# Kernel optimization log

Measured on AMD Instinct MI355X. Metric: run time of the kernel, lower is better.

## Reference

```python
import jax, jax.numpy as jnp
import numpy as np

N, C_IN, C_OUT, H = 4096, 1024, 512, 4
D = C_OUT // H  # per-head output dim
TEMP = 1.0


def setup_inputs() -> dict:
    key = jax.random.key(0)
    ks = jax.random.split(key, 6)
    node_feats = jax.random.normal(ks[0], (N, C_IN), dtype=jnp.float32)
    # sparse 0/1 adjacency mask, avg degree ~ 0.02*N
    adj_matrix = jax.random.bernoulli(ks[1], 0.02, (N, N)).astype(jnp.float32)
    lim_w = np.sqrt(6.0 / (C_IN + D))
    lim_v = np.sqrt(6.0 / (D + 1))
    W = jax.random.uniform(ks[2], (H, C_IN, D), jnp.float32, -lim_w, lim_w)
    b = jnp.zeros((H, D), dtype=jnp.float32)
    v0 = jax.random.uniform(ks[3], (H, D), jnp.float32, -lim_v, lim_v)
    v1 = jax.random.uniform(ks[4], (H, D), jnp.float32, -lim_v, lim_v)
    return {"node_feats": node_feats, "adj_matrix": adj_matrix,
            "W": W, "b": b, "v0": v0, "v1": v1}


def reference(node_feats, adj_matrix, W, b, v0, v1):
    # per-head linear projection: [H, N, D]
    h = jnp.einsum('nc,hcd->hnd', node_feats, W) + b[:, None, :]
    f1 = jnp.einsum('hnd,hd->hn', h, v0)  # [H, N]
    f2 = jnp.einsum('hnd,hd->hn', h, v1)  # [H, N]
    logits = adj_matrix[None, :, :] * (f1[:, :, None] + f2[:, None, :])
    # torch to_sparse drops exact zeros; sparse.softmax normalizes over
    # the remaining (nonzero) entries only, zeros stay zero when densified.
    mask = logits != 0
    vals = (jax.nn.sigmoid(logits) - 0.5) / TEMP
    rowmax = jnp.max(jnp.where(mask, vals, -1e30), axis=-1, keepdims=True)
    e = jnp.where(mask, jnp.exp(vals - rowmax), 0.0)
    denom = jnp.sum(e, axis=-1, keepdims=True)
    p = jnp.where(denom > 0, e / jnp.maximum(denom, 1e-30), 0.0)
    out = jnp.einsum('hnm,hmd->hnd', p, h)  # [H, N, D]
    # concat heads along feature dim -> [N, H*D]
    return out.transpose(1, 0, 2).reshape(node_feats.shape[0], -1)
```

## Files before the change

### kernel.cpp

```cpp
#include <hip/hip_runtime.h>
#include <hip/hip_bf16.h>

#define N_NODES 4096
#define C_IN    1024
#define H_HEADS 4
#define D_HEAD  128
#define C_OUT   512
#define DEG_CAP 256

typedef __attribute__((ext_vector_type(8))) short short8;
typedef __attribute__((ext_vector_type(8))) unsigned short u16x8;
typedef __attribute__((ext_vector_type(4))) float f32x4;

__device__ __forceinline__ unsigned short f2bf(float f) {
    unsigned u = __float_as_uint(f);
    u += 0x7FFFu + ((u >> 16) & 1u);
    return (unsigned short)(u >> 16);
}
__device__ __forceinline__ float bf2f(unsigned short u) {
    return __uint_as_float((unsigned)u << 16);
}
__device__ __forceinline__ float sigv(float s) {
    return 1.f / (1.f + __expf(-s)) - 0.5f;
}

#define GLOAD_LDS16(gp, lp)                                                        \
    __builtin_amdgcn_global_load_lds(                                              \
        (const __attribute__((address_space(1))) unsigned int*)(gp),               \
        (__attribute__((address_space(3))) unsigned int*)(lp), 16, 0, 0)

__global__ void k_xb(const float* __restrict__ X, unsigned short* __restrict__ Xb) {
    int g = blockIdx.x * blockDim.x + threadIdx.x;
    const float4* s = (const float4*)(X + (size_t)g * 8);
    float4 a = s[0], b = s[1];
    ushort4 p0, p1;
    p0.x = f2bf(a.x); p0.y = f2bf(a.y); p0.z = f2bf(a.z); p0.w = f2bf(a.w);
    p1.x = f2bf(b.x); p1.y = f2bf(b.y); p1.z = f2bf(b.z); p1.w = f2bf(b.w);
    ushort4* d = (ushort4*)(Xb + (size_t)g * 8);
    d[0] = p0; d[1] = p1;
}

__global__ void k_wt(const float* __restrict__ W, unsigned short* __restrict__ Wt) {
    int g = blockIdx.x * blockDim.x + threadIdx.x;
    int o = g * 4;
    int c  = o & 1023;
    int hd = o >> 10;
    int d  = hd & 127;
    int h  = hd >> 7;
    const float* src = W + (size_t)h * C_IN * D_HEAD + (size_t)c * D_HEAD + d;
    ushort4 p;
    p.x = f2bf(src[0 * D_HEAD]);
    p.y = f2bf(src[1 * D_HEAD]);
    p.z = f2bf(src[2 * D_HEAD]);
    p.w = f2bf(src[3 * D_HEAD]);
    *(ushort4*)(Wt + o) = p;
}

__global__ void k_gemm(const unsigned short* __restrict__ Xb,
                       const unsigned short* __restrict__ Wt,
                       const float* __restrict__ bias, unsigned short* __restrict__ Hb) {
    __shared__ __align__(16) unsigned short ldsA[2 * 64 * 32];
    __shared__ __align__(16) unsigned short ldsB[2 * 64 * 32];
    const int t    = threadIdx.x;
    const int lane = t & 63;
    const int wid  = t >> 6;
    const int wrow = wid >> 1, wcol = wid & 1;
    const int bid  = blockIdx.x;
    const int lin  = (bid & 7) * 64 + (bid >> 3);
    const int rowStart = (lin >> 3) * 64;
    const int colStart = (lin & 7) * 64;

    f32x4 acc[2][2];
#pragma unroll
    for (int m = 0; m < 2; ++m)
#pragma unroll
        for (int n = 0; n < 2; ++n) acc[m][n] = (f32x4){0.f, 0.f, 0.f, 0.f};

    const int lrow = lane >> 2;
    const int lkq  = lane & 3;

    for (int k0 = 0; k0 < C_IN; k0 += 64) {
#pragma unroll
        for (int i = 0; i < 2; ++i) {
            int c  = wid * 2 + i;
            int h  = c >> 2, rb = c & 3;
            const unsigned short* g =
                Xb + (size_t)(rowStart + rb * 16 + lrow) * C_IN + k0 + h * 32 + lkq * 8;
            GLOAD_LDS16(g, ldsA + h * 2048 + rb * 512);
        }
#pragma unroll
        for (int i = 0; i < 2; ++i) {
            int c  = wid * 2 + i;
            int h  = c >> 2, db = c & 3;
            const unsigned short* g =
                Wt + (size_t)(colStart + db * 16 + lrow) * C_IN + k0 + h * 32 + lkq * 8;
            GLOAD_LDS16(g, ldsB + h * 2048 + db * 512);
        }
        __syncthreads();

        const int fo = (lane >> 4) * 8;
        const int fr = lane & 15;
#pragma unroll
        for (int h = 0; h < 2; ++h) {
            short8 bfr[2];
#pragma unroll
            for (int n = 0; n < 2; ++n)
                bfr[n] = *(const short8*)(ldsB + h * 2048 + (wcol * 32 + n * 16 + fr) * 32 + fo);
#pragma unroll
            for (int m = 0; m < 2; ++m) {
                short8 a = *(const short8*)(ldsA + h * 2048 + (wrow * 32 + m * 16 + fr) * 32 + fo);
#pragma unroll
                for (int n = 0; n < 2; ++n)
                    acc[m][n] = __builtin_amdgcn_mfma_f32_16x16x32_bf16(a, bfr[n], acc[m][n], 0, 0, 0);
            }
        }
        __syncthreads();
    }

#pragma unroll
    for (int m = 0; m < 2; ++m) {
        int row_g = rowStart + wrow * 32 + m * 16 + (lane >> 4) * 4;
#pragma unroll
        for (int n = 0; n < 2; ++n) {
            int col_g = colStart + wcol * 32 + n * 16 + (lane & 15);
            float bb = bias[col_g];
#pragma unroll
            for (int r = 0; r < 4; ++r)
                Hb[(size_t)(row_g + r) * C_OUT + col_g] = f2bf(acc[m][n][r] + bb);
        }
    }
}

__global__ void k_prep(const float* __restrict__ adj, const unsigned short* __restrict__ Hb,
                       const float* __restrict__ v0, const float* __restrict__ v1,
                       float* __restrict__ F1, float* __restrict__ F2,
                       unsigned short* __restrict__ idx, int* __restrict__ nnz) {
    __shared__ int wtot[4];
    const int i    = blockIdx.x;
    const int t    = threadIdx.x;
    const int lane = t & 63;
    const int wid  = t >> 6;

    const float4* arow = (const float4*)(adj + (size_t)i * N_NODES);
    float4 av[4];
#pragma unroll
    for (int r = 0; r < 4; ++r) av[r] = arow[r * 256 + t];

    int c = 2 * t;
    unsigned int hp = *(const unsigned int*)(Hb + (size_t)i * C_OUT + c);
    float h0 = bf2f((unsigned short)(hp & 0xFFFFu));
    float h1 = bf2f((unsigned short)(hp >> 16));
    float s1 = h0 * v0[c] + h1 * v0[c + 1];
    float s2 = h0 * v1[c] + h1 * v1[c + 1];
#pragma unroll
    for (int off = 32; off; off >>= 1) {
        s1 += __shfl_xor(s1, off);
        s2 += __shfl_xor(s2, off);
    }
    if (lane == 0) {
        F1[i * 4 + wid] = s1;
        F2[i * 4 + wid] = s2;
    }

    int cnt = 0;
#pragma unroll
    for (int r = 0; r < 4; ++r)
        cnt += (av[r].x != 0.f) + (av[r].y != 0.f) + (av[r].z != 0.f) + (av[r].w != 0.f);
    int v = cnt;
#pragma unroll
    for (int off = 1; off < 64; off <<= 1) {
        int u = __shfl_up(v, off);
        if (lane >= off) v += u;
    }
    if (lane == 63) wtot[wid] = v;
    __syncthreads();
    int wpre = 0, total = 0;
#pragma unroll
    for (int w = 0; w < 4; ++w) {
        int tw = wtot[w];
        if (w < wid) wpre += tw;
        total += tw;
    }
    int off = wpre + v - cnt;
    unsigned short* ir = idx + (size_t)i * DEG_CAP;
#pragma unroll
    for (int r = 0; r < 4; ++r) {
        int j0 = (r * 256 + t) * 4;
        if (av[r].x != 0.f) { if (off < DEG_CAP) ir[off] = (unsigned short)j0;       off++; }
        if (av[r].y != 0.f) { if (off < DEG_CAP) ir[off] = (unsigned short)(j0 + 1); off++; }
        if (av[r].z != 0.f) { if (off < DEG_CAP) ir[off] = (unsigned short)(j0 + 2); off++; }
        if (av[r].w != 0.f) { if (off < DEG_CAP) ir[off] = (unsigned short)(j0 + 3); off++; }
    }
    if (t == 0) nnz[i] = min(total, DEG_CAP);
}

__global__ void k_pv(const unsigned short* __restrict__ idx, const int* __restrict__ nnz,
                     const float* __restrict__ F1, const float* __restrict__ F2,
                     const unsigned short* __restrict__ Hb, float* __restrict__ Out) {
    __shared__ unsigned short jl[DEG_CAP];
    __shared__ float ev[DEG_CAP * 4];
    __shared__ float partial[4][C_OUT];
    __shared__ float dred[4][4];
    const int i    = blockIdx.x;
    const int t    = threadIdx.x;
    const int lane = t & 63;
    const int wid  = t >> 6;
    const int headl = lane >> 4;

    const int nv = nnz[i];
    float4 f1v = *(const float4*)(F1 + i * 4);
    const unsigned short* __restrict__ ji = idx + (size_t)i * DEG_CAP;

    float d0 = 0.f, d1 = 0.f, d2 = 0.f, d3 = 0.f;
    for (int jj = t; jj < nv; jj += 256) {
        int j = ji[jj];
        jl[jj] = (unsigned short)j;
        float4 f2v = *(const float4*)(F2 + j * 4);
        float s0 = f1v.x + f2v.x, s1 = f1v.y + f2v.y;
        float s2 = f1v.z + f2v.z, s3 = f1v.w + f2v.w;
        float e0 = (s0 != 0.f) ? __expf(sigv(s0)) : 0.f;
        float e1 = (s1 != 0.f) ? __expf(sigv(s1)) : 0.f;
        float e2 = (s2 != 0.f) ? __expf(sigv(s2)) : 0.f;
        float e3 = (s3 != 0.f) ? __expf(sigv(s3)) : 0.f;
        ev[jj * 4 + 0] = e0; ev[jj * 4 + 1] = e1;
        ev[jj * 4 + 2] = e2; ev[jj * 4 + 3] = e3;
        d0 += e0; d1 += e1; d2 += e2; d3 += e3;
    }
#pragma unroll
    for (int o2 = 32; o2; o2 >>= 1) {
        d0 += __shfl_xor(d0, o2); d1 += __shfl_xor(d1, o2);
        d2 += __shfl_xor(d2, o2); d3 += __shfl_xor(d3, o2);
    }
    if (lane == 0) {
        dred[wid][0] = d0; dred[wid][1] = d1; dred[wid][2] = d2; dred[wid][3] = d3;
    }
    __syncthreads();

    float acc0[8], acc1[8];
#pragma unroll
    for (int k = 0; k < 8; ++k) { acc0[k] = 0.f; acc1[k] = 0.f; }
    const unsigned short* __restrict__ hp = Hb + lane * 8;

    int jj = wid;
#pragma unroll 4
    for (; jj + 4 < nv; jj += 8) {
        int ja = jl[jj], jb = jl[jj + 4];
        float ea = ev[jj * 4 + headl];
        float eb = ev[(jj + 4) * 4 + headl];
        u16x8 ha = *(const u16x8*)(hp + (size_t)ja * C_OUT);
        u16x8 hb = *(const u16x8*)(hp + (size_t)jb * C_OUT);
#pragma unroll
        for (int k = 0; k < 8; ++k) acc0[k] += ea * bf2f(ha[k]);
#pragma unroll
        for (int k = 0; k < 8; ++k) acc1[k] += eb * bf2f(hb[k]);
    }
    if (jj < nv) {
        int ja = jl[jj];
        float ea = ev[jj * 4 + headl];
        u16x8 ha = *(const u16x8*)(hp + (size_t)ja * C_OUT);
#pragma unroll
        for (int k = 0; k < 8; ++k) acc0[k] += ea * bf2f(ha[k]);
    }

    f32x4 lo = {acc0[0] + acc1[0], acc0[1] + acc1[1], acc0[2] + acc1[2], acc0[3] + acc1[3]};
    f32x4 hi = {acc0[4] + acc1[4], acc0[5] + acc1[5], acc0[6] + acc1[6], acc0[7] + acc1[7]};
    *(f32x4*)&partial[wid][lane * 8]     = lo;
    *(f32x4*)&partial[wid][lane * 8 + 4] = hi;
    __syncthreads();

    int head = t >> 6;
    float dn = dred[0][head] + dred[1][head] + dred[2][head] + dred[3][head];
    int c = 2 * t;
    float s0 = partial[0][c] + partial[1][c] + partial[2][c] + partial[3][c];
    float s1 = partial[0][c + 1] + partial[1][c + 1] + partial[2][c + 1] + partial[3][c + 1];
    float2 o;
    if (dn > 0.f) {
        float inv = 1.f / fmaxf(dn, 1e-30f);
        o.x = s0 * inv;
        o.y = s1 * inv;
    } else {
        o.x = 0.f; o.y = 0.f;
    }
    *(float2*)(Out + (size_t)i * C_OUT + c) = o;
}

extern "C" void kernel_launch(void* const* d_in, const int* in_sizes, int n_in,
                              void* d_out, int out_size, void* d_ws, size_t ws_size,
                              hipStream_t stream) {
    const float* X   = (const float*)d_in[0];
    const float* adj = (const float*)d_in[1];
    const float* W   = (const float*)d_in[2];
    const float* b   = (const float*)d_in[3];
    const float* v0  = (const float*)d_in[4];
    const float* v1  = (const float*)d_in[5];
    float* out = (float*)d_out;

    char* ws = (char*)d_ws;
    unsigned short* Wt  = (unsigned short*)ws;
    unsigned short* Xb  = (unsigned short*)(ws + (size_t)1 * 1024 * 1024);
    unsigned short* Hb  = (unsigned short*)(ws + (size_t)9 * 1024 * 1024);
    float*          F1  = (float*)(ws + (size_t)13 * 1024 * 1024);
    float*          F2  = F1 + N_NODES * 4;
    unsigned short* idx = (unsigned short*)(ws + (size_t)14 * 1024 * 1024);
    int*            nnz = (int*)(ws + (size_t)16 * 1024 * 1024);

    k_xb<<<2048, 256, 0, stream>>>(X, Xb);
    k_wt<<<512, 256, 0, stream>>>(W, Wt);
    k_gemm<<<512, 256, 0, stream>>>(Xb, Wt, b, Hb);
    k_prep<<<N_NODES, 256, 0, stream>>>(adj, Hb, v0, v1, F1, F2, idx, nnz);
    k_pv<<<N_NODES, 256, 0, stream>>>(idx, nnz, F1, F2, Hb, out);
}
```

Before: 60.83 us.

## Fuse adjacency compaction into attention kernel, merge conversions, double-buffer GEMM

Merges the X and W bf16 conversion kernels into one launch. Adds LDS double-buffering to the GEMM so the next K tile is prefetched while MFMAs run on the current one. Moves the adjacency-row scan and index compaction from the prep kernel into the attention kernel, keeping the indices in shared memory so no idx/nnz round-trip through global memory is needed. F1/F2 get their own small kernel with one row per wave. The risk is that the attention kernel now also streams the large adjacency matrix, which raises its per-block latency, and the edge-weight loop now assumes a degree of at most 256.

```diff
diff --git a/kernel.cpp b/kernel.cpp
--- a/kernel.cpp
+++ b/kernel.cpp
@@ -29,38 +29,39 @@
         (const __attribute__((address_space(1))) unsigned int*)(gp),               \
         (__attribute__((address_space(3))) unsigned int*)(lp), 16, 0, 0)
 
-__global__ void k_xb(const float* __restrict__ X, unsigned short* __restrict__ Xb) {
-    int g = blockIdx.x * blockDim.x + threadIdx.x;
-    const float4* s = (const float4*)(X + (size_t)g * 8);
-    float4 a = s[0], b = s[1];
-    ushort4 p0, p1;
-    p0.x = f2bf(a.x); p0.y = f2bf(a.y); p0.z = f2bf(a.z); p0.w = f2bf(a.w);
-    p1.x = f2bf(b.x); p1.y = f2bf(b.y); p1.z = f2bf(b.z); p1.w = f2bf(b.w);
-    ushort4* d = (ushort4*)(Xb + (size_t)g * 8);
-    d[0] = p0; d[1] = p1;
-}
-
-__global__ void k_wt(const float* __restrict__ W, unsigned short* __restrict__ Wt) {
-    int g = blockIdx.x * blockDim.x + threadIdx.x;
-    int o = g * 4;
-    int c  = o & 1023;
-    int hd = o >> 10;
-    int d  = hd & 127;
-    int h  = hd >> 7;
-    const float* src = W + (size_t)h * C_IN * D_HEAD + (size_t)c * D_HEAD + d;
-    ushort4 p;
-    p.x = f2bf(src[0 * D_HEAD]);
-    p.y = f2bf(src[1 * D_HEAD]);
-    p.z = f2bf(src[2 * D_HEAD]);
-    p.w = f2bf(src[3 * D_HEAD]);
-    *(ushort4*)(Wt + o) = p;
+__global__ void k_cvt(const float* __restrict__ X, const float* __restrict__ W,
+                      unsigned short* __restrict__ Xb, unsigned short* __restrict__ Wt) {
+    if (blockIdx.x < 2048) {
+        int g = blockIdx.x * blockDim.x + threadIdx.x;
+        const float4* s = (const float4*)(X + (size_t)g * 8);
+        float4 a = s[0], b = s[1];
+        ushort4 p0, p1;
+        p0.x = f2bf(a.x); p0.y = f2bf(a.y); p0.z = f2bf(a.z); p0.w = f2bf(a.w);
+        p1.x = f2bf(b.x); p1.y = f2bf(b.y); p1.z = f2bf(b.z); p1.w = f2bf(b.w);
+        ushort4* d = (ushort4*)(Xb + (size_t)g * 8);
+        d[0] = p0; d[1] = p1;
+    } else {
+        int g = (blockIdx.x - 2048) * blockDim.x + threadIdx.x;
+        int o = g * 4;
+        int c  = o & 1023;
+        int hd = o >> 10;
+        int d  = hd & 127;
+        int h  = hd >> 7;
+        const float* src = W + (size_t)h * C_IN * D_HEAD + (size_t)c * D_HEAD + d;
+        ushort4 p;
+        p.x = f2bf(src[0 * D_HEAD]);
+        p.y = f2bf(src[1 * D_HEAD]);
+        p.z = f2bf(src[2 * D_HEAD]);
+        p.w = f2bf(src[3 * D_HEAD]);
+        *(ushort4*)(Wt + o) = p;
+    }
 }
 
 __global__ void k_gemm(const unsigned short* __restrict__ Xb,
                        const unsigned short* __restrict__ Wt,
                        const float* __restrict__ bias, unsigned short* __restrict__ Hb) {
-    __shared__ __align__(16) unsigned short ldsA[2 * 64 * 32];
-    __shared__ __align__(16) unsigned short ldsB[2 * 64 * 32];
+    __shared__ __align__(16) unsigned short ldsA[2 * 64 * 64];
+    __shared__ __align__(16) unsigned short ldsB[2 * 64 * 64];
     const int t    = threadIdx.x;
     const int lane = t & 63;
     const int wid  = t >> 6;
@@ -79,42 +80,51 @@
     const int lrow = lane >> 2;
     const int lkq  = lane & 3;
 
-    for (int k0 = 0; k0 < C_IN; k0 += 64) {
-#pragma unroll
-        for (int i = 0; i < 2; ++i) {
-            int c  = wid * 2 + i;
+    auto stage = [&](int buf, int k0) {
+#pragma unroll
+        for (int ii = 0; ii < 2; ++ii) {
+            int c  = wid * 2 + ii;
             int h  = c >> 2, rb = c & 3;
             const unsigned short* g =
                 Xb + (size_t)(rowStart + rb * 16 + lrow) * C_IN + k0 + h * 32 + lkq * 8;
-            GLOAD_LDS16(g, ldsA + h * 2048 + rb * 512);
+            GLOAD_LDS16(g, ldsA + buf * 4096 + h * 2048 + rb * 512);
         }
 #pragma unroll
-        for (int i = 0; i < 2; ++i) {
-            int c  = wid * 2 + i;
+        for (int ii = 0; ii < 2; ++ii) {
+            int c  = wid * 2 + ii;
             int h  = c >> 2, db = c & 3;
             const unsigned short* g =
                 Wt + (size_t)(colStart + db * 16 + lrow) * C_IN + k0 + h * 32 + lkq * 8;
-            GLOAD_LDS16(g, ldsB + h * 2048 + db * 512);
+            GLOAD_LDS16(g, ldsB + buf * 4096 + h * 2048 + db * 512);
         }
-        __syncthreads();
-
-        const int fo = (lane >> 4) * 8;
-        const int fr = lane & 15;
+    };
+
+    stage(0, 0);
+    __syncthreads();
+
+    const int fo = (lane >> 4) * 8;
+    const int fr = lane & 15;
+    int cur = 0;
+    for (int kt = 0; kt < 16; ++kt) {
+        if (kt < 15) stage(cur ^ 1, (kt + 1) * 64);
+        const unsigned short* __restrict__ lA = ldsA + cur * 4096;
+        const unsigned short* __restrict__ lB = ldsB + cur * 4096;
 #pragma unroll
         for (int h = 0; h < 2; ++h) {
             short8 bfr[2];
 #pragma unroll
             for (int n = 0; n < 2; ++n)
-                bfr[n] = *(const short8*)(ldsB + h * 2048 + (wcol * 32 + n * 16 + fr) * 32 + fo);
+                bfr[n] = *(const short8*)(lB + h * 2048 + (wcol * 32 + n * 16 + fr) * 32 + fo);
 #pragma unroll
             for (int m = 0; m < 2; ++m) {
-                short8 a = *(const short8*)(ldsA + h * 2048 + (wrow * 32 + m * 16 + fr) * 32 + fo);
+                short8 a = *(const short8*)(lA + h * 2048 + (wrow * 32 + m * 16 + fr) * 32 + fo);
 #pragma unroll
                 for (int n = 0; n < 2; ++n)
                     acc[m][n] = __builtin_amdgcn_mfma_f32_16x16x32_bf16(a, bfr[n], acc[m][n], 0, 0, 0);
             }
         }
         __syncthreads();
+        cur ^= 1;
     }
 
 #pragma unroll
@@ -131,108 +141,109 @@
     }
 }
 
-__global__ void k_prep(const float* __restrict__ adj, const unsigned short* __restrict__ Hb,
-                       const float* __restrict__ v0, const float* __restrict__ v1,
-                       float* __restrict__ F1, float* __restrict__ F2,
-                       unsigned short* __restrict__ idx, int* __restrict__ nnz) {
-    __shared__ int wtot[4];
-    const int i    = blockIdx.x;
+__global__ void k_f12(const unsigned short* __restrict__ Hb, const float* __restrict__ v0,
+                      const float* __restrict__ v1, float* __restrict__ F1,
+                      float* __restrict__ F2) {
     const int t    = threadIdx.x;
     const int lane = t & 63;
     const int wid  = t >> 6;
-
-    const float4* arow = (const float4*)(adj + (size_t)i * N_NODES);
-    float4 av[4];
-#pragma unroll
-    for (int r = 0; r < 4; ++r) av[r] = arow[r * 256 + t];
-
-    int c = 2 * t;
-    unsigned int hp = *(const unsigned int*)(Hb + (size_t)i * C_OUT + c);
-    float h0 = bf2f((unsigned short)(hp & 0xFFFFu));
-    float h1 = bf2f((unsigned short)(hp >> 16));
-    float s1 = h0 * v0[c] + h1 * v0[c + 1];
-    float s2 = h0 * v1[c] + h1 * v1[c + 1];
-#pragma unroll
-    for (int off = 32; off; off >>= 1) {
+    const int row  = blockIdx.x * 4 + wid;
+    const int c0   = lane * 8;
+
+    u16x8 hv = *(const u16x8*)(Hb + (size_t)row * C_OUT + c0);
+    float4 va0 = *(const float4*)(v0 + c0), va1 = *(const float4*)(v0 + c0 + 4);
+    float4 vb0 = *(const float4*)(v1 + c0), vb1 = *(const float4*)(v1 + c0 + 4);
+    float h[8];
+#pragma unroll
+    for (int k = 0; k < 8; ++k) h[k] = bf2f(hv[k]);
+    float s1 = h[0]*va0.x + h[1]*va0.y + h[2]*va0.z + h[3]*va0.w
+             + h[4]*va1.x + h[5]*va1.y + h[6]*va1.z + h[7]*va1.w;
+    float s2 = h[0]*vb0.x + h[1]*vb0.y + h[2]*vb0.z + h[3]*vb0.w
+             + h[4]*vb1.x + h[5]*vb1.y + h[6]*vb1.z + h[7]*vb1.w;
+#pragma unroll
+    for (int off = 8; off; off >>= 1) {
         s1 += __shfl_xor(s1, off);
         s2 += __shfl_xor(s2, off);
     }
-    if (lane == 0) {
-        F1[i * 4 + wid] = s1;
-        F2[i * 4 + wid] = s2;
-    }
-
-    int cnt = 0;
-#pragma unroll
-    for (int r = 0; r < 4; ++r)
-        cnt += (av[r].x != 0.f) + (av[r].y != 0.f) + (av[r].z != 0.f) + (av[r].w != 0.f);
-    int v = cnt;
-#pragma unroll
-    for (int off = 1; off < 64; off <<= 1) {
-        int u = __shfl_up(v, off);
-        if (lane >= off) v += u;
-    }
-    if (lane == 63) wtot[wid] = v;
-    __syncthreads();
-    int wpre = 0, total = 0;
-#pragma unroll
-    for (int w = 0; w < 4; ++w) {
-        int tw = wtot[w];
-        if (w < wid) wpre += tw;
-        total += tw;
-    }
-    int off = wpre + v - cnt;
-    unsigned short* ir = idx + (size_t)i * DEG_CAP;
-#pragma unroll
-    for (int r = 0; r < 4; ++r) {
-        int j0 = (r * 256 + t) * 4;
-        if (av[r].x != 0.f) { if (off < DEG_CAP) ir[off] = (unsigned short)j0;       off++; }
-        if (av[r].y != 0.f) { if (off < DEG_CAP) ir[off] = (unsigned short)(j0 + 1); off++; }
-        if (av[r].z != 0.f) { if (off < DEG_CAP) ir[off] = (unsigned short)(j0 + 2); off++; }
-        if (av[r].w != 0.f) { if (off < DEG_CAP) ir[off] = (unsigned short)(j0 + 3); off++; }
-    }
-    if (t == 0) nnz[i] = min(total, DEG_CAP);
-}
-
-__global__ void k_pv(const unsigned short* __restrict__ idx, const int* __restrict__ nnz,
-                     const float* __restrict__ F1, const float* __restrict__ F2,
-                     const unsigned short* __restrict__ Hb, float* __restrict__ Out) {
+    if ((lane & 15) == 0) {
+        int head = lane >> 4;
+        F1[row * 4 + head] = s1;
+        F2[row * 4 + head] = s2;
+    }
+}
+
+__global__ void k_attn2(const float* __restrict__ adj, const unsigned short* __restrict__ Hb,
+                        const float* __restrict__ F1, const float* __restrict__ F2,
+                        float* __restrict__ Out) {
     __shared__ unsigned short jl[DEG_CAP];
     __shared__ float ev[DEG_CAP * 4];
     __shared__ float partial[4][C_OUT];
     __shared__ float dred[4][4];
+    __shared__ int   wtot[4];
+
     const int i    = blockIdx.x;
     const int t    = threadIdx.x;
     const int lane = t & 63;
     const int wid  = t >> 6;
     const int headl = lane >> 4;
 
-    const int nv = nnz[i];
+    const float4* arow = (const float4*)(adj + (size_t)i * N_NODES);
+    float4 av[4];
+#pragma unroll
+    for (int r = 0; r < 4; ++r) av[r] = arow[r * 256 + t];
     float4 f1v = *(const float4*)(F1 + i * 4);
-    const unsigned short* __restrict__ ji = idx + (size_t)i * DEG_CAP;
-
-    float d0 = 0.f, d1 = 0.f, d2 = 0.f, d3 = 0.f;
-    for (int jj = t; jj < nv; jj += 256) {
-        int j = ji[jj];
-        jl[jj] = (unsigned short)j;
+
+    int cnt = 0;
+#pragma unroll
+    for (int r = 0; r < 4; ++r)
+        cnt += (av[r].x != 0.f) + (av[r].y != 0.f) + (av[r].z != 0.f) + (av[r].w != 0.f);
+    int v = cnt;
+#pragma unroll
+    for (int off = 1; off < 64; off <<= 1) {
+        int u = __shfl_up(v, off);
+        if (lane >= off) v += u;
+    }
+    if (lane == 63) wtot[wid] = v;
+    __syncthreads();
+    int wpre = 0, total = 0;
+#pragma unroll
+    for (int w = 0; w < 4; ++w) {
+        int tw = wtot[w];
+        if (w < wid) wpre += tw;
+        total += tw;
+    }
+    const int nv = min(total, DEG_CAP);
+    int off = wpre + v - cnt;
+#pragma unroll
+    for (int r = 0; r < 4; ++r) {
+        int j0 = (r * 256 + t) * 4;
+        if (av[r].x != 0.f) { if (off < DEG_CAP) jl[off] = (unsigned short)j0;       off++; }
+        if (av[r].y != 0.f) { if (off < DEG_CAP) jl[off] = (unsigned short)(j0 + 1); off++; }
+        if (av[r].z != 0.f) { if (off < DEG_CAP) jl[off] = (unsigned short)(j0 + 2); off++; }
+        if (av[r].w != 0.f) { if (off < DEG_CAP) jl[off] = (unsigned short)(j0 + 3); off++; }
+    }
+    __syncthreads();
+
+    float e0 = 0.f, e1 = 0.f, e2 = 0.f, e3 = 0.f;
+    if (t < nv) {
+        int j = jl[t];
         float4 f2v = *(const float4*)(F2 + j * 4);
         float s0 = f1v.x + f2v.x, s1 = f1v.y + f2v.y;
         float s2 = f1v.z + f2v.z, s3 = f1v.w + f2v.w;
-        float e0 = (s0 != 0.f) ? __expf(sigv(s0)) : 0.f;
-        float e1 = (s1 != 0.f) ? __expf(sigv(s1)) : 0.f;
-        float e2 = (s2 != 0.f) ? __expf(sigv(s2)) : 0.f;
-        float e3 = (s3 != 0.f) ? __expf(sigv(s3)) : 0.f;
-        ev[jj * 4 + 0] = e0; ev[jj * 4 + 1] = e1;
-        ev[jj * 4 + 2] = e2; ev[jj * 4 + 3] = e3;
-        d0 += e0; d1 += e1; d2 += e2; d3 += e3;
+        e0 = (s0 != 0.f) ? __expf(sigv(s0)) : 0.f;
+        e1 = (s1 != 0.f) ? __expf(sigv(s1)) : 0.f;
+        e2 = (s2 != 0.f) ? __expf(sigv(s2)) : 0.f;
+        e3 = (s3 != 0.f) ? __expf(sigv(s3)) : 0.f;
+        ev[t * 4 + 0] = e0; ev[t * 4 + 1] = e1;
+        ev[t * 4 + 2] = e2; ev[t * 4 + 3] = e3;
     }
 #pragma unroll
     for (int o2 = 32; o2; o2 >>= 1) {
-        d0 += __shfl_xor(d0, o2); d1 += __shfl_xor(d1, o2);
-        d2 += __shfl_xor(d2, o2); d3 += __shfl_xor(d3, o2);
+        e0 += __shfl_xor(e0, o2); e1 += __shfl_xor(e1, o2);
+        e2 += __shfl_xor(e2, o2); e3 += __shfl_xor(e3, o2);
     }
     if (lane == 0) {
-        dred[wid][0] = d0; dred[wid][1] = d1; dred[wid][2] = d2; dred[wid][3] = d3;
+        dred[wid][0] = e0; dred[wid][1] = e1; dred[wid][2] = e2; dred[wid][3] = e3;
     }
     __syncthreads();
 
@@ -301,12 +312,9 @@
     unsigned short* Hb  = (unsigned short*)(ws + (size_t)9 * 1024 * 1024);
     float*          F1  = (float*)(ws + (size_t)13 * 1024 * 1024);
     float*          F2  = F1 + N_NODES * 4;
-    unsigned short* idx = (unsigned short*)(ws + (size_t)14 * 1024 * 1024);
-    int*            nnz = (int*)(ws + (size_t)16 * 1024 * 1024);
-
-    k_xb<<<2048, 256, 0, stream>>>(X, Xb);
-    k_wt<<<512, 256, 0, stream>>>(W, Wt);
+
+    k_cvt<<<2560, 256, 0, stream>>>(X, W, Xb, Wt);
     k_gemm<<<512, 256, 0, stream>>>(Xb, Wt, b, Hb);
-    k_prep<<<N_NODES, 256, 0, stream>>>(adj, Hb, v0, v1, F1, F2, idx, nnz);
-    k_pv<<<N_NODES, 256, 0, stream>>>(idx, nnz, F1, F2, Hb, out);
-}
+    k_f12<<<N_NODES / 4, 256, 0, stream>>>(Hb, v0, v1, F1, F2);
+    k_attn2<<<N_NODES, 256, 0, stream>>>(adj, Hb, F1, F2, out);
+}
```

Measured after the change: 61.68 us. No clear change (+1.4%).
